# Performance work log

Hardware: AMD Instinct MI355X
Metric: run time of the kernel (lower is better)

## Reference

```python
import jax, jax.numpy as jnp
import numpy as np

B, S, D, H = 4, 2048, 1024, 16
HD = D // H  # head dim = 64
EPS = 1e-12


def setup_inputs() -> dict:
    key = jax.random.key(0)
    ks = jax.random.split(key, 9)
    sc = 1.0 / np.sqrt(D)
    return {
        "X": jax.random.normal(ks[0], (B, S, D), jnp.float32),
        "Wq": jax.random.normal(ks[1], (D, D), jnp.float32) * sc,
        "bq": jnp.zeros((D,), jnp.float32),
        "Wk": jax.random.normal(ks[2], (D, D), jnp.float32) * sc,
        "bk": jnp.zeros((D,), jnp.float32),
        "Wv": jax.random.normal(ks[3], (D, D), jnp.float32) * sc,
        "bv": jnp.zeros((D,), jnp.float32),
        "Wo": jax.random.normal(ks[4], (D, D), jnp.float32) * sc,
        "bo": jnp.zeros((D,), jnp.float32),
        "gamma": jnp.ones((D,), jnp.float32),
        "beta": jnp.zeros((D,), jnp.float32),
    }


def _attention_block(X, Wq, bq, Wk, bk, Wv, bv, Wo, bo, gamma, beta):
    def heads(t):  # [B,S,D] -> [B,H,S,HD]
        return t.reshape(B, S, H, HD).transpose(0, 2, 1, 3)

    Q = heads(X @ Wq.T + bq)
    K = heads(X @ Wk.T + bk)
    V = heads(X @ Wv.T + bv)
    A = jnp.einsum("bhqd,bhkd->bhqk", Q, K) / np.sqrt(HD)
    A = jax.nn.softmax(A, axis=-1)
    O = jnp.einsum("bhqk,bhkd->bhqd", A, V)
    O = O.transpose(0, 2, 1, 3).reshape(B, S, D)
    O = O @ Wo.T + bo
    Y = O + X
    mu = Y.mean(-1, keepdims=True)
    var = jnp.square(Y - mu).mean(-1, keepdims=True)
    return gamma * (Y - mu) / jnp.sqrt(var + EPS) + beta


def reference(X, Wq, bq, Wk, bk, Wv, bv, Wo, bo, gamma, beta):
    return _attention_block(X, Wq, bq, Wk, bk, Wv, bv, Wo, bo, gamma, beta)
```

## Files before the change

kernel.cpp:

```cpp
#include <hip/hip_runtime.h>
#include <hip/hip_bf16.h>

#define B_ 4
#define S_ 2048
#define D_ 1024
#define H_ 16
#define HD_ 64
#define M_ (B_*S_)
#define BH_ (B_*H_)

typedef __bf16 bf16;
typedef __attribute__((ext_vector_type(8))) __bf16 bf16x8;
typedef __attribute__((ext_vector_type(4))) __bf16 bf16x4;
typedef __attribute__((ext_vector_type(4))) float f32x4;
typedef __attribute__((ext_vector_type(16))) float f32x16;
typedef __attribute__((ext_vector_type(4))) unsigned u32x4;

#define MFMA16(a,b,c) __builtin_amdgcn_mfma_f32_16x16x32_bf16((a),(b),(c),0,0,0)
#define MFMA32(a,b,c) __builtin_amdgcn_mfma_f32_32x32x16_bf16((a),(b),(c),0,0,0)

__device__ __forceinline__ void gl2lds16(const void* g, void* l) {
  __builtin_amdgcn_global_load_lds(
      (__attribute__((address_space(1))) void*)(g),
      (__attribute__((address_space(3))) void*)(l), 16, 0, 0);
}

__device__ __forceinline__ float fexp2(float x) {
  float r;
  asm("v_exp_f32 %0, %1" : "=v"(r) : "v"(x));
  return r;
}

__device__ __forceinline__ unsigned cvtpk(float lo, float hi) {
  unsigned r;
  asm("v_cvt_pk_bf16_f32 %0, %1, %2" : "=v"(r) : "v"(lo), "v"(hi));
  return r;
}


__global__ __launch_bounds__(256) void k_cvt_t(const float* __restrict__ in,
                                               bf16* __restrict__ out, int nrow) {
  const int u = blockIdx.x * 256 + threadIdx.x;
  if (u >= nrow * 128) return;
  const int m = u >> 7, kc = u & 127;
  f32x4 v0 = *(const f32x4*)(in + (size_t)m * D_ + kc * 8);
  f32x4 v1 = *(const f32x4*)(in + (size_t)m * D_ + kc * 8 + 4);
  bf16x8 o;
  o[0]=(bf16)v0[0]; o[1]=(bf16)v0[1]; o[2]=(bf16)v0[2]; o[3]=(bf16)v0[3];
  o[4]=(bf16)v1[0]; o[5]=(bf16)v1[1]; o[6]=(bf16)v1[2]; o[7]=(bf16)v1[3];
  const int yt = m >> 7, kt = kc >> 3;
  const int f = ((m >> 4) & 7) * 2 + ((kc >> 2) & 1);
  const int lane = (kc & 3) * 16 + (m & 15);
  *(bf16x8*)&out[((size_t)(yt * 16 + kt) * 16 + f) * 512 + lane * 8] = o;
}

__global__ __launch_bounds__(512, 4) void k_gemm_qkv(
    const bf16* __restrict__ At, const bf16* __restrict__ Wt,
    const float* __restrict__ bq, const float* __restrict__ bk,
    const float* __restrict__ bvp,
    bf16* __restrict__ Qb, bf16* __restrict__ Kb, bf16* __restrict__ Vt,
    float scl_q) {
  __shared__ __align__(16) bf16 As[2][16 * 512];
  __shared__ __align__(16) bf16 Bs[2][16 * 512];
  const int t = threadIdx.x;
  const int l = t & 63, w = t >> 6;
  const int g = l >> 4, c = l & 15;
  const int wm = w >> 2, wn = w & 3;

  const int bid = blockIdx.x;
  const int lg = (bid & 7) * 192 + (bid >> 3);
  const int xt = lg % 24, yt = lg / 24;
  const int m0 = yt * 128;

  const bf16* Ab = At + (size_t)yt * 8192 * 16;
  const bf16* Bb = Wt + (size_t)xt * 8192 * 16;

  f32x4 acc[4][2];
#pragma unroll
  for (int i = 0; i < 4; ++i)
#pragma unroll
    for (int j = 0; j < 2; ++j) acc[i][j] = (f32x4)(0.0f);

#define STG(buf, kt)                                                          \
  do {                                                                        \
    for (int p = 0; p < 2; ++p) {                                             \
      const int f = p * 8 + w;                                                \
      gl2lds16(Ab + (size_t)(kt) * 8192 + f * 512 + l * 8, &As[buf][f * 512]);\
      gl2lds16(Bb + (size_t)(kt) * 8192 + f * 512 + l * 8, &Bs[buf][f * 512]);\
    }                                                                         \
  } while (0)

  STG(0, 0);
  __syncthreads();

  for (int kt = 0; kt < D_ / 64; ++kt) {
    const int cur = kt & 1;
    if (kt + 1 < D_ / 64) STG(cur ^ 1, kt + 1);
#pragma unroll
    for (int kk = 0; kk < 2; ++kk) {
      bf16x8 af[4], bw[2];
#pragma unroll
      for (int i = 0; i < 4; ++i)
        af[i] = *(const bf16x8*)&As[cur][(((wm * 4 + i) * 2 + kk) * 512) + l * 8];
#pragma unroll
      for (int j = 0; j < 2; ++j)
        bw[j] = *(const bf16x8*)&Bs[cur][(((wn * 2 + j) * 2 + kk) * 512) + l * 8];
#pragma unroll
      for (int i = 0; i < 4; ++i)
#pragma unroll
        for (int j = 0; j < 2; ++j) acc[i][j] = MFMA16(af[i], bw[j], acc[i][j]);
    }
    __syncthreads();
  }
#undef STG

  const int sec = xt >> 3;
  const int nbase = (xt & 7) * 128 + wn * 32;
  const float* bptr = (sec == 0) ? bq : (sec == 1) ? bk : bvp;
  const float scl = (sec == 0) ? scl_q : 1.0f;

  float bvj[2];
#pragma unroll
  for (int j = 0; j < 2; ++j) bvj[j] = bptr[nbase + j * 16 + c];

#pragma unroll
  for (int i = 0; i < 4; ++i) {
#pragma unroll
    for (int j = 0; j < 2; ++j) {
#pragma unroll
      for (int r = 0; r < 4; ++r) {
        const int m = m0 + wm * 64 + i * 16 + g * 4 + r;
        const int n = nbase + j * 16 + c;
        const float v = (acc[i][j][r] + bvj[j]) * scl;
        const int b = m >> 11, s = m & (S_ - 1);
        const int h = n >> 6, hd = n & 63;
        const size_t hb = ((size_t)(b * H_ + h)) * S_ * HD_;
        if (sec == 0) {
          Qb[hb + (size_t)s * HD_ + hd] = (bf16)v;
        } else if (sec == 1) {
          const int f = (hd >> 4) * 2 + ((s >> 5) & 1);
          const int lane = (s & 31) + ((hd >> 3) & 1) * 32;
          Kb[hb + (s >> 6) * 4096 + f * 512 + lane * 8 + (hd & 7)] = (bf16)v;
        } else {
          const int sl = s & 63;
          const int f = (sl >> 4) * 2 + (hd >> 5);
          const int lane = (hd & 31) + ((sl >> 3) & 1) * 32;
          Vt[hb + (s >> 6) * 4096 + f * 512 + lane * 8 + (sl & 7)] = (bf16)v;
        }
      }
    }
  }
}

__global__ __launch_bounds__(512, 4) void k_gemm_o(
    const bf16* __restrict__ At, const bf16* __restrict__ Wt,
    const float* __restrict__ bias, const float* __restrict__ Xres,
    float* __restrict__ Yb) {
  __shared__ __align__(16) bf16 As[2][16 * 512];
  __shared__ __align__(16) bf16 Bs[2][16 * 512];
  const int t = threadIdx.x;
  const int l = t & 63, w = t >> 6;
  const int g = l >> 4, c = l & 15;
  const int wm = w >> 2, wn = w & 3;

  const int bid = blockIdx.x;
  const int lg = (bid & 7) * 64 + (bid >> 3);
  const int xt = lg & 7, yt = lg >> 3;
  const int m0 = yt * 128, n0 = xt * 128;

  const bf16* Ab = At + (size_t)yt * 8192 * 16;
  const bf16* Bb = Wt + (size_t)xt * 8192 * 16;

  f32x4 acc[4][2];
#pragma unroll
  for (int i = 0; i < 4; ++i)
#pragma unroll
    for (int j = 0; j < 2; ++j) acc[i][j] = (f32x4)(0.0f);

#define STG(buf, kt)                                                          \
  do {                                                                        \
    for (int p = 0; p < 2; ++p) {                                             \
      const int f = p * 8 + w;                                                \
      gl2lds16(Ab + (size_t)(kt) * 8192 + f * 512 + l * 8, &As[buf][f * 512]);\
      gl2lds16(Bb + (size_t)(kt) * 8192 + f * 512 + l * 8, &Bs[buf][f * 512]);\
    }                                                                         \
  } while (0)

  STG(0, 0);
  __syncthreads();

  for (int kt = 0; kt < D_ / 64; ++kt) {
    const int cur = kt & 1;
    if (kt + 1 < D_ / 64) STG(cur ^ 1, kt + 1);
#pragma unroll
    for (int kk = 0; kk < 2; ++kk) {
      bf16x8 af[4], bw[2];
#pragma unroll
      for (int i = 0; i < 4; ++i)
        af[i] = *(const bf16x8*)&As[cur][(((wm * 4 + i) * 2 + kk) * 512) + l * 8];
#pragma unroll
      for (int j = 0; j < 2; ++j)
        bw[j] = *(const bf16x8*)&Bs[cur][(((wn * 2 + j) * 2 + kk) * 512) + l * 8];
#pragma unroll
      for (int i = 0; i < 4; ++i)
#pragma unroll
        for (int j = 0; j < 2; ++j) acc[i][j] = MFMA16(af[i], bw[j], acc[i][j]);
    }
    __syncthreads();
  }
#undef STG

  float bvj[2];
#pragma unroll
  for (int j = 0; j < 2; ++j) bvj[j] = bias[n0 + wn * 32 + j * 16 + c];

#pragma unroll
  for (int i = 0; i < 4; ++i) {
#pragma unroll
    for (int j = 0; j < 2; ++j) {
#pragma unroll
      for (int r = 0; r < 4; ++r) {
        const int m = m0 + wm * 64 + i * 16 + g * 4 + r;
        const int n = n0 + wn * 32 + j * 16 + c;
        Yb[(size_t)m * D_ + n] =
            acc[i][j][r] + bvj[j] + Xres[(size_t)m * D_ + n];
      }
    }
  }
}

__global__ __launch_bounds__(256, 4) void k_attn(const bf16* __restrict__ Q,
                                                 const bf16* __restrict__ Kb,
                                                 const bf16* __restrict__ Vt,
                                                 bf16* __restrict__ Obt) {
  __shared__ __align__(16) bf16 Ks[2][8 * 512];
  __shared__ __align__(16) bf16 Vs[2][8 * 512];
  const int t = threadIdx.x;
  const int l = t & 63, w = t >> 6;
  const int c32 = l & 31, hi = l >> 5;

  const int bid = blockIdx.x;
  const int lg = (bid & 7) * 128 + (bid >> 3);
  const int bh = lg >> 4;
  const int q0 = (lg & 15) * 128 + w * 32;

  const bf16* Qh = Q + (size_t)bh * S_ * HD_;
  const bf16* Kt = Kb + (size_t)bh * S_ * HD_;
  const bf16* Vb = Vt + (size_t)bh * S_ * HD_;

  bf16x8 qf[4];
#pragma unroll
  for (int kk = 0; kk < 4; ++kk)
    qf[kk] = *(const bf16x8*)&Qh[(size_t)(q0 + c32) * HD_ + kk * 16 + hi * 8];

  f32x16 acc0 = (f32x16)(0.f), acc1 = (f32x16)(0.f);
  float m_c = -__builtin_inff(), l_c = 0.f;

#define STGA(buf, kt)                                                         \
  do {                                                                        \
    for (int p = 0; p < 2; ++p) {                                             \
      const int f = p * 4 + w;                                                \
      gl2lds16(Kt + (size_t)(kt) * 4096 + f * 512 + l * 8, &Ks[buf][f * 512]);\
      gl2lds16(Vb + (size_t)(kt) * 4096 + f * 512 + l * 8, &Vs[buf][f * 512]);\
    }                                                                         \
  } while (0)

  STGA(0, 0);
  __syncthreads();

  for (int kt = 0; kt < S_ / 64; ++kt) {
    const int cur = kt & 1;
    if (kt + 1 < S_ / 64) STGA(cur ^ 1, kt + 1);

    f32x16 st0 = (f32x16)(0.f), st1 = (f32x16)(0.f);
    __builtin_amdgcn_s_setprio(1);
#pragma unroll
    for (int kk = 0; kk < 4; ++kk) {
      bf16x8 kf0 = *(const bf16x8*)&Ks[cur][(kk * 2) * 512 + l * 8];
      bf16x8 kf1 = *(const bf16x8*)&Ks[cur][(kk * 2 + 1) * 512 + l * 8];
      st0 = MFMA32(kf0, qf[kk], st0);
      st1 = MFMA32(kf1, qf[kk], st1);
    }
    __builtin_amdgcn_s_setprio(0);

    float tm;
    {
      f32x16 mx;
#pragma unroll
      for (int r = 0; r < 16; ++r) mx[r] = fmaxf(st0[r], st1[r]);
      float m8[8];
#pragma unroll
      for (int r = 0; r < 8; ++r) m8[r] = fmaxf(mx[r], mx[r + 8]);
      float m4[4];
#pragma unroll
      for (int r = 0; r < 4; ++r) m4[r] = fmaxf(m8[r], m8[r + 4]);
      tm = fmaxf(fmaxf(m4[0], m4[1]), fmaxf(m4[2], m4[3]));
      tm = fmaxf(tm, __shfl_xor(tm, 32));
    }
    if (!__all(tm <= m_c + 8.f)) {
      const float mn = fmaxf(m_c, tm);
      const float cf = fexp2(m_c - mn);
      m_c = mn;
      l_c *= cf;
#pragma unroll
      for (int r = 0; r < 16; ++r) { acc0[r] *= cf; acc1[r] *= cf; }
    }
    float rs = 0.f;
#pragma unroll
    for (int r = 0; r < 16; ++r) { st0[r] = fexp2(st0[r] - m_c); rs += st0[r]; }
#pragma unroll
    for (int r = 0; r < 16; ++r) { st1[r] = fexp2(st1[r] - m_c); rs += st1[r]; }
    rs += __shfl_xor(rs, 32);
    l_c += rs;

    unsigned ca[8], cb[8];
#pragma unroll
    for (int i = 0; i < 8; ++i) {
      ca[i] = cvtpk(st0[2 * i], st0[2 * i + 1]);
      cb[i] = cvtpk(st1[2 * i], st1[2 * i + 1]);
    }
    asm volatile("v_permlane32_swap_b32 %0, %1" : "+v"(ca[0]), "+v"(ca[2]));
    asm volatile("v_permlane32_swap_b32 %0, %1" : "+v"(ca[1]), "+v"(ca[3]));
    asm volatile("v_permlane32_swap_b32 %0, %1" : "+v"(ca[4]), "+v"(ca[6]));
    asm volatile("v_permlane32_swap_b32 %0, %1" : "+v"(ca[5]), "+v"(ca[7]));
    asm volatile("v_permlane32_swap_b32 %0, %1" : "+v"(cb[0]), "+v"(cb[2]));
    asm volatile("v_permlane32_swap_b32 %0, %1" : "+v"(cb[1]), "+v"(cb[3]));
    asm volatile("v_permlane32_swap_b32 %0, %1" : "+v"(cb[4]), "+v"(cb[6]));
    asm volatile("v_permlane32_swap_b32 %0, %1" : "+v"(cb[5]), "+v"(cb[7]));
    bf16x8 pf[4];
    pf[0] = __builtin_bit_cast(bf16x8, (u32x4){ca[0], ca[1], ca[2], ca[3]});
    pf[1] = __builtin_bit_cast(bf16x8, (u32x4){ca[4], ca[5], ca[6], ca[7]});
    pf[2] = __builtin_bit_cast(bf16x8, (u32x4){cb[0], cb[1], cb[2], cb[3]});
    pf[3] = __builtin_bit_cast(bf16x8, (u32x4){cb[4], cb[5], cb[6], cb[7]});

    __builtin_amdgcn_s_setprio(1);
#pragma unroll
    for (int kb = 0; kb < 4; ++kb) {
      bf16x8 vf0 = *(const bf16x8*)&Vs[cur][(kb * 2) * 512 + l * 8];
      bf16x8 vf1 = *(const bf16x8*)&Vs[cur][(kb * 2 + 1) * 512 + l * 8];
      acc0 = MFMA32(vf0, pf[kb], acc0);
      acc1 = MFMA32(vf1, pf[kb], acc1);
    }
    __builtin_amdgcn_s_setprio(0);

    __syncthreads();
  }
#undef STGA

  const float li = 1.f / l_c;
  const int b = bh >> 4, h = bh & 15;
  const int m = b * S_ + q0 + c32;
  const int yt2 = m >> 7, rb = (m >> 4) & 7, c16 = m & 15;
  bf16* tb = Obt + ((size_t)(yt2 * 16 + h) * 16) * 512;
#pragma unroll
  for (int rq = 0; rq < 4; ++rq) {
    bf16x4 o0, o1;
#pragma unroll
    for (int j = 0; j < 4; ++j) {
      o0[j] = (bf16)(acc0[rq * 4 + j] * li);
      o1[j] = (bf16)(acc1[rq * 4 + j] * li);
    }
    const int lo = (rq * 16 + c16) * 8 + hi * 4;
    *(bf16x4*)&tb[(rb * 2 + 0) * 512 + lo] = o0;
    *(bf16x4*)&tb[(rb * 2 + 1) * 512 + lo] = o1;
  }
}

__global__ __launch_bounds__(256) void k_ln(const float* __restrict__ Y,
                                            const float* __restrict__ gamma,
                                            const float* __restrict__ beta,
                                            float* __restrict__ out) {
  __shared__ float red[8];
  const int row = blockIdx.x, t = threadIdx.x;
  const float* y = Y + (size_t)row * D_;
  f32x4 v = *(const f32x4*)(y + t * 4);
  float s = v[0] + v[1] + v[2] + v[3];
  float s2 = v[0]*v[0] + v[1]*v[1] + v[2]*v[2] + v[3]*v[3];
#pragma unroll
  for (int mk = 1; mk <= 32; mk <<= 1) {
    s += __shfl_xor(s, mk);
    s2 += __shfl_xor(s2, mk);
  }
  if ((t & 63) == 0) { red[t >> 6] = s; red[4 + (t >> 6)] = s2; }
  __syncthreads();
  const float ts = red[0] + red[1] + red[2] + red[3];
  const float ts2 = red[4] + red[5] + red[6] + red[7];
  const float mu = ts * (1.0f / D_);
  const float inv = rsqrtf(ts2 * (1.0f / D_) - mu * mu + 1e-12f);
  f32x4 gm = *(const f32x4*)(gamma + t * 4);
  f32x4 bt = *(const f32x4*)(beta + t * 4);
  f32x4 o;
#pragma unroll
  for (int j = 0; j < 4; ++j) o[j] = gm[j] * (v[j] - mu) * inv + bt[j];
  *(f32x4*)(out + (size_t)row * D_ + t * 4) = o;
}

extern "C" void kernel_launch(void* const* d_in, const int* in_sizes, int n_in,
                              void* d_out, int out_size, void* d_ws, size_t ws_size,
                              hipStream_t stream) {
  const float* X     = (const float*)d_in[0];
  const float* Wq    = (const float*)d_in[1];
  const float* bq    = (const float*)d_in[2];
  const float* Wk    = (const float*)d_in[3];
  const float* bk    = (const float*)d_in[4];
  const float* Wv    = (const float*)d_in[5];
  const float* bv    = (const float*)d_in[6];
  const float* Wo    = (const float*)d_in[7];
  const float* bo    = (const float*)d_in[8];
  const float* gamma = (const float*)d_in[9];
  const float* beta  = (const float*)d_in[10];

  char* ws = (char*)d_ws;
  bf16* Xt  = (bf16*)(ws + 0);
  bf16* Wct = (bf16*)(ws + (16u << 20));
  bf16* Wot = (bf16*)(ws + (22u << 20));
  bf16* Qb  = (bf16*)(ws + (24u << 20));
  bf16* Kb  = (bf16*)(ws + (40u << 20));
  bf16* Vt  = (bf16*)(ws + (56u << 20));
  bf16* Obt = (bf16*)(ws + (72u << 20));
  float* Yb = (float*)(ws + (88u << 20));

  const float SCL = 0.125f * 1.44269504088896340736f;
  const size_t WSZ = (size_t)D_ * D_;

  k_cvt_t<<<M_ * 128 / 256, 256, 0, stream>>>(X, Xt, M_);
  k_cvt_t<<<D_ * 128 / 256, 256, 0, stream>>>(Wq, Wct, D_);
  k_cvt_t<<<D_ * 128 / 256, 256, 0, stream>>>(Wk, Wct + WSZ, D_);
  k_cvt_t<<<D_ * 128 / 256, 256, 0, stream>>>(Wv, Wct + 2 * WSZ, D_);
  k_cvt_t<<<D_ * 128 / 256, 256, 0, stream>>>(Wo, Wot, D_);

  k_gemm_qkv<<<1536, 512, 0, stream>>>(Xt, Wct, bq, bk, bv, Qb, Kb, Vt, SCL);
  k_attn<<<1024, 256, 0, stream>>>(Qb, Kb, Vt, Obt);
  k_gemm_o<<<512, 512, 0, stream>>>(Obt, Wot, bo, X, Yb);
  k_ln<<<M_, 256, 0, stream>>>(Yb, gamma, beta, (float*)d_out);
}
```

Baseline: 323.5 us.

## Single-buffer GEMM LDS staging and compute softmax row sums via MFMA

Both projection GEMMs drop LDS double buffering and load each K tile synchronously before computing, which halves LDS use and may raise occupancy but loses overlap of global loads with MFMA work. The attention kernel removes the per-tile scalar row-sum reduction and its cross-lane shuffle. Instead it accumulates the softmax denominator with an extra MFMA against a vector of ones, using the bf16-rounded probabilities. The max reduction is also reshaped into a three-way tree. The extra MFMA per key block adds matrix-unit work in exchange for fewer VALU adds and shuffles.

New measurement: 304.2 us. 1.06x faster.

```diff
diff --git a/kernel.cpp b/kernel.cpp
--- a/kernel.cpp
+++ b/kernel.cpp
@@ -60,8 +60,8 @@
     const float* __restrict__ bvp,
     bf16* __restrict__ Qb, bf16* __restrict__ Kb, bf16* __restrict__ Vt,
     float scl_q) {
-  __shared__ __align__(16) bf16 As[2][16 * 512];
-  __shared__ __align__(16) bf16 Bs[2][16 * 512];
+  __shared__ __align__(16) bf16 As[16 * 512];
+  __shared__ __align__(16) bf16 Bs[16 * 512];
   const int t = threadIdx.x;
   const int l = t & 63, w = t >> 6;
   const int g = l >> 4, c = l & 15;
@@ -81,30 +81,23 @@
 #pragma unroll
     for (int j = 0; j < 2; ++j) acc[i][j] = (f32x4)(0.0f);
 
-#define STG(buf, kt)                                                          \
-  do {                                                                        \
-    for (int p = 0; p < 2; ++p) {                                             \
-      const int f = p * 8 + w;                                                \
-      gl2lds16(Ab + (size_t)(kt) * 8192 + f * 512 + l * 8, &As[buf][f * 512]);\
-      gl2lds16(Bb + (size_t)(kt) * 8192 + f * 512 + l * 8, &Bs[buf][f * 512]);\
-    }                                                                         \
-  } while (0)
-
-  STG(0, 0);
-  __syncthreads();
-
   for (int kt = 0; kt < D_ / 64; ++kt) {
-    const int cur = kt & 1;
-    if (kt + 1 < D_ / 64) STG(cur ^ 1, kt + 1);
+#pragma unroll
+    for (int p = 0; p < 2; ++p) {
+      const int f = p * 8 + w;
+      gl2lds16(Ab + (size_t)kt * 8192 + f * 512 + l * 8, &As[f * 512]);
+      gl2lds16(Bb + (size_t)kt * 8192 + f * 512 + l * 8, &Bs[f * 512]);
+    }
+    __syncthreads();
 #pragma unroll
     for (int kk = 0; kk < 2; ++kk) {
       bf16x8 af[4], bw[2];
 #pragma unroll
       for (int i = 0; i < 4; ++i)
-        af[i] = *(const bf16x8*)&As[cur][(((wm * 4 + i) * 2 + kk) * 512) + l * 8];
+        af[i] = *(const bf16x8*)&As[(((wm * 4 + i) * 2 + kk) * 512) + l * 8];
 #pragma unroll
       for (int j = 0; j < 2; ++j)
-        bw[j] = *(const bf16x8*)&Bs[cur][(((wn * 2 + j) * 2 + kk) * 512) + l * 8];
+        bw[j] = *(const bf16x8*)&Bs[(((wn * 2 + j) * 2 + kk) * 512) + l * 8];
 #pragma unroll
       for (int i = 0; i < 4; ++i)
 #pragma unroll
@@ -112,7 +105,6 @@
     }
     __syncthreads();
   }
-#undef STG
 
   const int sec = xt >> 3;
   const int nbase = (xt & 7) * 128 + wn * 32;
@@ -156,8 +148,8 @@
     const bf16* __restrict__ At, const bf16* __restrict__ Wt,
     const float* __restrict__ bias, const float* __restrict__ Xres,
     float* __restrict__ Yb) {
-  __shared__ __align__(16) bf16 As[2][16 * 512];
-  __shared__ __align__(16) bf16 Bs[2][16 * 512];
+  __shared__ __align__(16) bf16 As[16 * 512];
+  __shared__ __align__(16) bf16 Bs[16 * 512];
   const int t = threadIdx.x;
   const int l = t & 63, w = t >> 6;
   const int g = l >> 4, c = l & 15;
@@ -177,30 +169,23 @@
 #pragma unroll
     for (int j = 0; j < 2; ++j) acc[i][j] = (f32x4)(0.0f);
 
-#define STG(buf, kt)                                                          \
-  do {                                                                        \
-    for (int p = 0; p < 2; ++p) {                                             \
-      const int f = p * 8 + w;                                                \
-      gl2lds16(Ab + (size_t)(kt) * 8192 + f * 512 + l * 8, &As[buf][f * 512]);\
-      gl2lds16(Bb + (size_t)(kt) * 8192 + f * 512 + l * 8, &Bs[buf][f * 512]);\
-    }                                                                         \
-  } while (0)
-
-  STG(0, 0);
-  __syncthreads();
-
   for (int kt = 0; kt < D_ / 64; ++kt) {
-    const int cur = kt & 1;
-    if (kt + 1 < D_ / 64) STG(cur ^ 1, kt + 1);
+#pragma unroll
+    for (int p = 0; p < 2; ++p) {
+      const int f = p * 8 + w;
+      gl2lds16(Ab + (size_t)kt * 8192 + f * 512 + l * 8, &As[f * 512]);
+      gl2lds16(Bb + (size_t)kt * 8192 + f * 512 + l * 8, &Bs[f * 512]);
+    }
+    __syncthreads();
 #pragma unroll
     for (int kk = 0; kk < 2; ++kk) {
       bf16x8 af[4], bw[2];
 #pragma unroll
       for (int i = 0; i < 4; ++i)
-        af[i] = *(const bf16x8*)&As[cur][(((wm * 4 + i) * 2 + kk) * 512) + l * 8];
+        af[i] = *(const bf16x8*)&As[(((wm * 4 + i) * 2 + kk) * 512) + l * 8];
 #pragma unroll
       for (int j = 0; j < 2; ++j)
-        bw[j] = *(const bf16x8*)&Bs[cur][(((wn * 2 + j) * 2 + kk) * 512) + l * 8];
+        bw[j] = *(const bf16x8*)&Bs[(((wn * 2 + j) * 2 + kk) * 512) + l * 8];
 #pragma unroll
       for (int i = 0; i < 4; ++i)
 #pragma unroll
@@ -208,7 +193,6 @@
     }
     __syncthreads();
   }
-#undef STG
 
   float bvj[2];
 #pragma unroll
@@ -253,8 +237,12 @@
   for (int kk = 0; kk < 4; ++kk)
     qf[kk] = *(const bf16x8*)&Qh[(size_t)(q0 + c32) * HD_ + kk * 16 + hi * 8];
 
-  f32x16 acc0 = (f32x16)(0.f), acc1 = (f32x16)(0.f);
-  float m_c = -__builtin_inff(), l_c = 0.f;
+  bf16x8 onesf;
+#pragma unroll
+  for (int i = 0; i < 8; ++i) onesf[i] = (bf16)1.0f;
+
+  f32x16 acc0 = (f32x16)(0.f), acc1 = (f32x16)(0.f), accl = (f32x16)(0.f);
+  float m_c = -__builtin_inff();
 
 #define STGA(buf, kt)                                                         \
   do {                                                                        \
@@ -285,33 +273,36 @@
 
     float tm;
     {
-      f32x16 mx;
-#pragma unroll
-      for (int r = 0; r < 16; ++r) mx[r] = fmaxf(st0[r], st1[r]);
-      float m8[8];
-#pragma unroll
-      for (int r = 0; r < 8; ++r) m8[r] = fmaxf(mx[r], mx[r + 8]);
-      float m4[4];
-#pragma unroll
-      for (int r = 0; r < 4; ++r) m4[r] = fmaxf(m8[r], m8[r + 4]);
-      tm = fmaxf(fmaxf(m4[0], m4[1]), fmaxf(m4[2], m4[3]));
-      tm = fmaxf(tm, __shfl_xor(tm, 32));
+      float a0 = fmaxf(fmaxf(st0[0], st0[1]), st0[2]);
+      float a1 = fmaxf(fmaxf(st0[3], st0[4]), st0[5]);
+      float a2 = fmaxf(fmaxf(st0[6], st0[7]), st0[8]);
+      float a3 = fmaxf(fmaxf(st0[9], st0[10]), st0[11]);
+      float a4 = fmaxf(fmaxf(st0[12], st0[13]), st0[14]);
+      float a5 = fmaxf(fmaxf(st0[15], st1[0]), st1[1]);
+      float a6 = fmaxf(fmaxf(st1[2], st1[3]), st1[4]);
+      float a7 = fmaxf(fmaxf(st1[5], st1[6]), st1[7]);
+      float a8 = fmaxf(fmaxf(st1[8], st1[9]), st1[10]);
+      float a9 = fmaxf(fmaxf(st1[11], st1[12]), st1[13]);
+      float a10 = fmaxf(st1[14], st1[15]);
+      float b0 = fmaxf(fmaxf(a0, a1), a2);
+      float b1 = fmaxf(fmaxf(a3, a4), a5);
+      float b2 = fmaxf(fmaxf(a6, a7), a8);
+      float b3 = fmaxf(a9, a10);
+      float cx = fmaxf(fmaxf(b0, b1), fmaxf(b2, b3));
+      tm = fmaxf(cx, __shfl_xor(cx, 32));
     }
     if (!__all(tm <= m_c + 8.f)) {
       const float mn = fmaxf(m_c, tm);
       const float cf = fexp2(m_c - mn);
       m_c = mn;
-      l_c *= cf;
+      accl[0] *= cf;
 #pragma unroll
       for (int r = 0; r < 16; ++r) { acc0[r] *= cf; acc1[r] *= cf; }
     }
-    float rs = 0.f;
-#pragma unroll
-    for (int r = 0; r < 16; ++r) { st0[r] = fexp2(st0[r] - m_c); rs += st0[r]; }
-#pragma unroll
-    for (int r = 0; r < 16; ++r) { st1[r] = fexp2(st1[r] - m_c); rs += st1[r]; }
-    rs += __shfl_xor(rs, 32);
-    l_c += rs;
+#pragma unroll
+    for (int r = 0; r < 16; ++r) st0[r] = fexp2(st0[r] - m_c);
+#pragma unroll
+    for (int r = 0; r < 16; ++r) st1[r] = fexp2(st1[r] - m_c);
 
     unsigned ca[8], cb[8];
 #pragma unroll
@@ -340,6 +331,7 @@
       bf16x8 vf1 = *(const bf16x8*)&Vs[cur][(kb * 2 + 1) * 512 + l * 8];
       acc0 = MFMA32(vf0, pf[kb], acc0);
       acc1 = MFMA32(vf1, pf[kb], acc1);
+      accl = MFMA32(onesf, pf[kb], accl);
     }
     __builtin_amdgcn_s_setprio(0);
 
@@ -347,7 +339,7 @@
   }
 #undef STGA
 
-  const float li = 1.f / l_c;
+  const float li = 1.f / accl[0];
   const int b = bh >> 4, h = bh & 15;
   const int m = b * S_ + q0 + c32;
   const int yt2 = m >> 7, rb = (m >> 4) & 7, c16 = m & 15;
```
